# Kernel tuning notes

Measured on AMD Instinct MI355X. Metric: run time of the kernel, lower is better.

Reference implementation:

```python
import jax, jax.numpy as jnp
import numpy as np

B = 128
N = 512            # num_nodes
RU = 64            # rnn_units = hidden_size // num_nodes
IN_PER_NODE = 2    # input_size // num_nodes
MEM_DIM = 16
BOT_DIM = 4
IN_SZ = IN_PER_NODE + RU      # 66, concat(input, state) per node
OUT_SZ = 4 * RU               # 256, 4 LSTM gates


def setup_inputs() -> dict:
    key = jax.random.key(0)
    ks = jax.random.split(key, 12)
    std = 1.0 / np.sqrt(N * RU)  # reset_parameters: uniform(-std, std)
    u = lambda k, shape: jax.random.uniform(k, shape, jnp.float32, -std, std)
    return {
        "inputs": jax.random.normal(ks[0], (B, N * IN_PER_NODE), jnp.float32),
        "hx": jax.random.normal(ks[1], (B, N * RU), jnp.float32),
        "cx": jax.random.normal(ks[2], (B, N * RU), jnp.float32),
        "memory": u(ks[3], (N, MEM_DIM)),
        "w1": u(ks[4], (MEM_DIM, MEM_DIM)),
        "b1": u(ks[5], (MEM_DIM,)),
        "w2": u(ks[6], (MEM_DIM, BOT_DIM)),
        "b2": u(ks[7], (BOT_DIM,)),
        "w3": u(ks[8], (BOT_DIM, IN_SZ * OUT_SZ)),
        "b3": u(ks[9], (IN_SZ * OUT_SZ,)),
        "b_out": u(ks[10], (OUT_SZ,)),
    }


def reference(inputs, hx, cx, memory, w1, b1, w2, b2, w3, b3, b_out):
    b = inputs.shape[0]
    n = memory.shape[0]
    ru = hx.shape[1] // n
    # per-node concat of input and state: [B, N, IN_SZ]
    x = inputs.reshape(b, n, -1)
    h = hx.reshape(b, n, ru)
    xs = jnp.concatenate([x, h], axis=-1)
    # hypernetwork: memory -> per-node weight matrices [N, IN_SZ, OUT_SZ]
    mem = jnp.tanh(memory @ w1 + b1)
    mem = jnp.tanh(mem @ w2 + b2)
    W = (mem @ w3 + b3).reshape(n, xs.shape[-1], -1)
    # batched per-node matmul (original repeats W over batch; same math without the repeat)
    val = jax.nn.sigmoid(jnp.einsum('bni,nio->bno', xs, W)) + b_out  # [B, N, 4*RU]
    g = val.reshape(b, n, 4, ru)
    i_t = jax.nn.sigmoid(g[:, :, 0, :].reshape(b, n * ru))
    f_t = jax.nn.sigmoid(g[:, :, 1, :].reshape(b, n * ru))
    g_t = jnp.tanh(g[:, :, 2, :].reshape(b, n * ru))
    o_t = jax.nn.sigmoid(g[:, :, 3, :].reshape(b, n * ru))
    cy = cx * f_t + i_t * g_t
    hy = o_t * jnp.tanh(cy)
    return hy, cy
```

## Files before the change

### kernel.cpp

```cpp
#include <hip/hip_runtime.h>
#include <math.h>

#define BATCH 128
#define NNODE 512
#define RU 64
#define MEM_DIM 16
#define BOT_DIM 4
#define IN_SZ 66
#define OUT_SZ 256
#define HID (NNODE*RU)
#define W3_ROW 16896
#define W5F_FLOATS (240*512)
#define K_STEP 24576

typedef __attribute__((ext_vector_type(8))) short short8;
typedef __attribute__((ext_vector_type(4))) float float4v;

__device__ __forceinline__ unsigned short f2bf(float f) {
    unsigned int u = __float_as_uint(f);
    unsigned int r = (u + 0x7FFFu + ((u >> 16) & 1u)) >> 16;
    return (unsigned short)r;
}
__device__ __forceinline__ float fsig(float x) {
    return __builtin_amdgcn_rcpf(1.0f + __expf(-x));
}
__device__ __forceinline__ float ftanh(float x) {
    return 1.0f - 2.0f * __builtin_amdgcn_rcpf(1.0f + __expf(2.0f * x));
}

__global__ __launch_bounds__(256) void prep_kernel(
    const float* __restrict__ memory, const float* __restrict__ w1,
    const float* __restrict__ b1,     const float* __restrict__ w2,
    const float* __restrict__ b2,     const float* __restrict__ w3,
    const float* __restrict__ b3,     float* __restrict__ W5f,
    float* __restrict__ m2_ws)
{
    const int tid = threadIdx.x;
    const int bid = blockIdx.x;
    if (bid < 120) {
        const int id = bid * 256 + tid;
        const int F  = id * 4;
        const int f  = F >> 9;
        const int r  = F & 511;
        const int lane = r >> 3;
        const int j0   = r & 7;
        const int ks = f % 3;
        const int t2 = f / 3;
        const int ct = t2 & 15;
        const int k  = t2 >> 4;
        const int q = lane & 15, quad = lane >> 4;
        const int o = (ct & 3) * 64 + (ct >> 2) * 16 + q;
        const float* src = (k < 4) ? (w3 + k * W3_ROW) : b3;
        float4v v;
        #pragma unroll
        for (int jj = 0; jj < 4; ++jj) {
            const int s = ks * 32 + quad * 8 + j0 + jj;
            float x = 0.f;
            if (s < IN_SZ) {
                const int i = (s < 64) ? s + 2 : s - 64;
                x = src[i * OUT_SZ + o];
            }
            v[jj] = x;
        }
        *(float4v*)(W5f + F) = v;
    } else {
        const int n = (bid - 120) * 256 + tid;
        if (n < NNODE) {
            float memv[MEM_DIM];
            #pragma unroll
            for (int j = 0; j < MEM_DIM; ++j) memv[j] = memory[n * MEM_DIM + j];
            float mem1[MEM_DIM];
            #pragma unroll
            for (int t = 0; t < MEM_DIM; ++t) {
                float s = b1[t];
                #pragma unroll
                for (int j = 0; j < MEM_DIM; ++j) s += memv[j] * w1[j * MEM_DIM + t];
                mem1[t] = ftanh(s);
            }
            #pragma unroll
            for (int t = 0; t < BOT_DIM; ++t) {
                float s = b2[t];
                #pragma unroll
                for (int j = 0; j < MEM_DIM; ++j) s += mem1[j] * w2[j * BOT_DIM + t];
                m2_ws[n * 4 + t] = ftanh(s);
            }
        }
    }
}

__global__ __launch_bounds__(256, 3) void fused_kernel(
    const float* __restrict__ inputs, const float* __restrict__ hx,
    const float* __restrict__ cx,     const float* __restrict__ b_out,
    const float* __restrict__ W5f,    const float* __restrict__ m2_ws,
    float* __restrict__ out)
{
    __shared__ unsigned short Wl[24 * 512];
    const int tid  = threadIdx.x;
    const unsigned bid = blockIdx.x;
    const int n    = bid >> 1;
    const int h    = bid & 1;
    const int w    = tid >> 6;
    const int lane = tid & 63;
    const int q    = lane & 15;
    const int quad = lane >> 4;

    float coef[4];
    #pragma unroll
    for (int k = 0; k < 4; ++k) coef[k] = m2_ws[n * 4 + k];

    float4v xa[2][4];
    float xin[2][2];
    #pragma unroll
    for (int rt = 0; rt < 2; ++rt) {
        const int row = w * 32 + rt * 16 + q;
        const float* hrow = hx + (size_t)row * HID + n * RU + quad * 8;
        xa[rt][0] = *(const float4v*)(hrow);
        xa[rt][1] = *(const float4v*)(hrow + 4);
        xa[rt][2] = *(const float4v*)(hrow + 32);
        xa[rt][3] = *(const float4v*)(hrow + 36);
        if (quad == 0) {
            const float* ip = inputs + (size_t)row * (NNODE * 2) + n * 2;
            xin[rt][0] = ip[0];
            xin[rt][1] = ip[1];
        } else {
            xin[rt][0] = 0.f;
            xin[rt][1] = 0.f;
        }
    }

    #pragma unroll
    for (int it = 0; it < 6; ++it) {
        const int c  = it * 256 + tid;
        const int fl = c >> 6;
        const int l  = c & 63;
        const int ctl = fl / 3;
        const int ks  = fl - ctl * 3;
        const float* p = W5f + (size_t)(((h * 8 + ctl) * 3 + ks) * 512) + l * 8;
        float4v r0 = *(const float4v*)(p + 4 * K_STEP);
        float4v r1 = *(const float4v*)(p + 4 * K_STEP + 4);
        #pragma unroll
        for (int k = 0; k < 4; ++k) {
            r0 += coef[k] * *(const float4v*)(p + k * K_STEP);
            r1 += coef[k] * *(const float4v*)(p + k * K_STEP + 4);
        }
        short8 ov;
        ov[0] = (short)f2bf(r0[0]); ov[1] = (short)f2bf(r0[1]);
        ov[2] = (short)f2bf(r0[2]); ov[3] = (short)f2bf(r0[3]);
        ov[4] = (short)f2bf(r1[0]); ov[5] = (short)f2bf(r1[1]);
        ov[6] = (short)f2bf(r1[2]); ov[7] = (short)f2bf(r1[3]);
        *(short8*)(Wl + fl * 512 + l * 8) = ov;
    }

    float bo[2][4];
    #pragma unroll
    for (int rh = 0; rh < 2; ++rh)
        #pragma unroll
        for (int g = 0; g < 4; ++g)
            bo[rh][g] = b_out[g * 64 + (h * 2 + rh) * 16 + q];

    float cxr[2][4][2];
    #pragma unroll
    for (int rt = 0; rt < 2; ++rt)
        #pragma unroll
        for (int v = 0; v < 4; ++v) {
            const int b = w * 32 + rt * 16 + quad * 4 + v;
            #pragma unroll
            for (int rh = 0; rh < 2; ++rh)
                cxr[rt][v][rh] = cx[(size_t)b * HID + n * RU + (h * 2 + rh) * 16 + q];
        }

    short8 a[3][2];
    #pragma unroll
    for (int rt = 0; rt < 2; ++rt) {
        #pragma unroll
        for (int ksh = 0; ksh < 2; ++ksh) {
            float4v lo = xa[rt][ksh * 2];
            float4v hi = xa[rt][ksh * 2 + 1];
            short8 t;
            t[0] = (short)f2bf(lo[0]); t[1] = (short)f2bf(lo[1]);
            t[2] = (short)f2bf(lo[2]); t[3] = (short)f2bf(lo[3]);
            t[4] = (short)f2bf(hi[0]); t[5] = (short)f2bf(hi[1]);
            t[6] = (short)f2bf(hi[2]); t[7] = (short)f2bf(hi[3]);
            a[ksh][rt] = t;
        }
        short8 t2 = {0, 0, 0, 0, 0, 0, 0, 0};
        t2[0] = (short)f2bf(xin[rt][0]);
        t2[1] = (short)f2bf(xin[rt][1]);
        a[2][rt] = t2;
    }

    float4v acc[2][8];
    #pragma unroll
    for (int rt = 0; rt < 2; ++rt)
        #pragma unroll
        for (int ctl = 0; ctl < 8; ++ctl)
            acc[rt][ctl] = (float4v){0.f, 0.f, 0.f, 0.f};

    __syncthreads();

    #pragma unroll
    for (int ks = 0; ks < 3; ++ks) {
        #pragma unroll
        for (int ctl = 0; ctl < 8; ++ctl) {
            short8 bf = *(const short8*)(Wl + (ctl * 3 + ks) * 512 + lane * 8);
            acc[0][ctl] = __builtin_amdgcn_mfma_f32_16x16x32_bf16(a[ks][0], bf, acc[0][ctl], 0, 0, 0);
            acc[1][ctl] = __builtin_amdgcn_mfma_f32_16x16x32_bf16(a[ks][1], bf, acc[1][ctl], 0, 0, 0);
        }
    }

    #pragma unroll
    for (int rt = 0; rt < 2; ++rt) {
        #pragma unroll
        for (int v = 0; v < 4; ++v) {
            const int b = w * 32 + rt * 16 + quad * 4 + v;
            const size_t base = (size_t)b * HID + n * RU;
            #pragma unroll
            for (int rh = 0; rh < 2; ++rh) {
                float vi = fsig(acc[rt][rh * 4 + 0][v]) + bo[rh][0];
                float vf = fsig(acc[rt][rh * 4 + 1][v]) + bo[rh][1];
                float vg = fsig(acc[rt][rh * 4 + 2][v]) + bo[rh][2];
                float vo = fsig(acc[rt][rh * 4 + 3][v]) + bo[rh][3];
                float it = fsig(vi), ft = fsig(vf);
                float gt = ftanh(vg), ot = fsig(vo);
                const size_t idx = base + (h * 2 + rh) * 16 + q;
                float cc = cxr[rt][v][rh] * ft + it * gt;
                out[idx] = ot * ftanh(cc);
                out[(size_t)BATCH * HID + idx] = cc;
            }
        }
    }
}

extern "C" void kernel_launch(void* const* d_in, const int* in_sizes, int n_in,
                              void* d_out, int out_size, void* d_ws, size_t ws_size,
                              hipStream_t stream) {
    const float* inputs = (const float*)d_in[0];
    const float* hx     = (const float*)d_in[1];
    const float* cx     = (const float*)d_in[2];
    const float* memory = (const float*)d_in[3];
    const float* w1     = (const float*)d_in[4];
    const float* b1     = (const float*)d_in[5];
    const float* w2     = (const float*)d_in[6];
    const float* b2     = (const float*)d_in[7];
    const float* w3     = (const float*)d_in[8];
    const float* b3     = (const float*)d_in[9];
    const float* b_out  = (const float*)d_in[10];
    float* out = (float*)d_out;

    float* W5f   = (float*)d_ws;
    float* m2_ws = (float*)((char*)d_ws + W5F_FLOATS * 4);

    prep_kernel<<<122, 256, 0, stream>>>(memory, w1, b1, w2, b2, w3, b3, W5f, m2_ws);
    fused_kernel<<<NNODE * 2, 256, 0, stream>>>(inputs, hx, cx, b_out, W5f, m2_ws, out);
}
```

Measured before the change: 126.8 us.

## Precompute per-node bf16 weights in a separate kernel and async-load into LDS

Moves the hypernetwork weight combination out of the GEMM kernel into a dedicated kernel. That kernel writes fully materialized per-node bf16 weight matrices (512 x 24576 bf16, about 25 MB) to the workspace. The GEMM kernel then streams its half-tile straight into LDS with global_load_lds, replacing the 5-way fp32 loads and FMAs it did per block. It also swaps the manual bf16 rounding for packed bf16x2 conversion intrinsics and drops the occupancy hint. The tradeoff is a large extra global write and read of materialized weights, where before each GEMM block recomputed them from a small shared table.

```diff
diff --git a/kernel.cpp b/kernel.cpp
--- a/kernel.cpp
+++ b/kernel.cpp
@@ -1,4 +1,5 @@
 #include <hip/hip_runtime.h>
+#include <hip/hip_bf16.h>
 #include <math.h>
 
 #define BATCH 128
@@ -10,16 +11,16 @@
 #define OUT_SZ 256
 #define HID (NNODE*RU)
 #define W3_ROW 16896
-#define W5F_FLOATS (240*512)
-#define K_STEP 24576
+#define NODE_WC 24576
+#define HALF_WC 12288
 
 typedef __attribute__((ext_vector_type(8))) short short8;
 typedef __attribute__((ext_vector_type(4))) float float4v;
 
-__device__ __forceinline__ unsigned short f2bf(float f) {
-    unsigned int u = __float_as_uint(f);
-    unsigned int r = (u + 0x7FFFu + ((u >> 16) & 1u)) >> 16;
-    return (unsigned short)r;
+__device__ __forceinline__ unsigned pack2(float x, float y) {
+    union { __hip_bfloat162 h; unsigned u; } cv;
+    cv.h = __float22bfloat162_rn(make_float2(x, y));
+    return cv.u;
 }
 __device__ __forceinline__ float fsig(float x) {
     return __builtin_amdgcn_rcpf(1.0f + __expf(-x));
@@ -28,73 +29,86 @@
     return 1.0f - 2.0f * __builtin_amdgcn_rcpf(1.0f + __expf(2.0f * x));
 }
 
-__global__ __launch_bounds__(256) void prep_kernel(
+__global__ __launch_bounds__(256) void wcomb_kernel(
     const float* __restrict__ memory, const float* __restrict__ w1,
     const float* __restrict__ b1,     const float* __restrict__ w2,
     const float* __restrict__ b2,     const float* __restrict__ w3,
-    const float* __restrict__ b3,     float* __restrict__ W5f,
-    float* __restrict__ m2_ws)
+    const float* __restrict__ b3,     unsigned short* __restrict__ Wc)
 {
+    __shared__ alignas(16) float w5s[2][5][512];
+    __shared__ float mem1s[16][MEM_DIM];
+    __shared__ float m2s[16][BOT_DIM];
+
     const int tid = threadIdx.x;
-    const int bid = blockIdx.x;
-    if (bid < 120) {
-        const int id = bid * 256 + tid;
-        const int F  = id * 4;
-        const int f  = F >> 9;
-        const int r  = F & 511;
-        const int lane = r >> 3;
-        const int j0   = r & 7;
+    const unsigned bid = blockIdx.x;
+    const int fp = bid >> 5;
+    const int ng = bid & 31;
+
+    for (int e = tid; e < 5120; e += 256) {
+        const int fl  = e / 2560;
+        const int k   = (e - fl * 2560) >> 9;
+        const int idx = e & 511;
+        const int l = idx >> 3, j = idx & 7;
+        const int f  = fp * 2 + fl;
         const int ks = f % 3;
-        const int t2 = f / 3;
-        const int ct = t2 & 15;
-        const int k  = t2 >> 4;
-        const int q = lane & 15, quad = lane >> 4;
+        const int ct = f / 3;
+        const int q = l & 15, quad = l >> 4;
         const int o = (ct & 3) * 64 + (ct >> 2) * 16 + q;
-        const float* src = (k < 4) ? (w3 + k * W3_ROW) : b3;
-        float4v v;
-        #pragma unroll
-        for (int jj = 0; jj < 4; ++jj) {
-            const int s = ks * 32 + quad * 8 + j0 + jj;
-            float x = 0.f;
-            if (s < IN_SZ) {
-                const int i = (s < 64) ? s + 2 : s - 64;
-                x = src[i * OUT_SZ + o];
-            }
-            v[jj] = x;
-        }
-        *(float4v*)(W5f + F) = v;
-    } else {
-        const int n = (bid - 120) * 256 + tid;
-        if (n < NNODE) {
-            float memv[MEM_DIM];
-            #pragma unroll
-            for (int j = 0; j < MEM_DIM; ++j) memv[j] = memory[n * MEM_DIM + j];
-            float mem1[MEM_DIM];
-            #pragma unroll
-            for (int t = 0; t < MEM_DIM; ++t) {
-                float s = b1[t];
-                #pragma unroll
-                for (int j = 0; j < MEM_DIM; ++j) s += memv[j] * w1[j * MEM_DIM + t];
-                mem1[t] = ftanh(s);
-            }
-            #pragma unroll
-            for (int t = 0; t < BOT_DIM; ++t) {
-                float s = b2[t];
-                #pragma unroll
-                for (int j = 0; j < MEM_DIM; ++j) s += mem1[j] * w2[j * BOT_DIM + t];
-                m2_ws[n * 4 + t] = ftanh(s);
-            }
-        }
-    }
-}
-
-__global__ __launch_bounds__(256, 3) void fused_kernel(
+        const int s = ks * 32 + quad * 8 + j;
+        float v = 0.f;
+        if (s < IN_SZ) {
+            const int i = (s < 64) ? s + 2 : s - 64;
+            v = (k < 4) ? w3[k * W3_ROW + i * OUT_SZ + o] : b3[i * OUT_SZ + o];
+        }
+        w5s[fl][k][idx] = v;
+    }
+
+    {
+        const int nn = tid >> 4, t = tid & 15;
+        float s = b1[t];
+        #pragma unroll
+        for (int j = 0; j < MEM_DIM; ++j)
+            s += memory[(ng * 16 + nn) * MEM_DIM + j] * w1[j * MEM_DIM + t];
+        mem1s[nn][t] = ftanh(s);
+    }
+    __syncthreads();
+    if (tid < 64) {
+        const int nn = tid >> 2, t4 = tid & 3;
+        float s = b2[t4];
+        #pragma unroll
+        for (int j = 0; j < MEM_DIM; ++j)
+            s += mem1s[nn][j] * w2[j * BOT_DIM + t4];
+        m2s[nn][t4] = ftanh(s);
+    }
+    __syncthreads();
+
+    const int fl   = tid >> 7;
+    const int idx4 = (tid & 127) * 4;
+    const float4v wk0 = *(const float4v*)&w5s[fl][0][idx4];
+    const float4v wk1 = *(const float4v*)&w5s[fl][1][idx4];
+    const float4v wk2 = *(const float4v*)&w5s[fl][2][idx4];
+    const float4v wk3 = *(const float4v*)&w5s[fl][3][idx4];
+    const float4v wb  = *(const float4v*)&w5s[fl][4][idx4];
+
+    unsigned short* base = Wc + (size_t)(ng * 16) * NODE_WC
+                         + (fp * 2 + fl) * 512 + idx4;
+    #pragma unroll 4
+    for (int nn = 0; nn < 16; ++nn) {
+        float4v r = wb + m2s[nn][0] * wk0 + m2s[nn][1] * wk1
+                       + m2s[nn][2] * wk2 + m2s[nn][3] * wk3;
+        uint2 p;
+        p.x = pack2(r[0], r[1]);
+        p.y = pack2(r[2], r[3]);
+        *(uint2*)(base + (size_t)nn * NODE_WC) = p;
+    }
+}
+
+__global__ __launch_bounds__(256) void gemm_kernel(
     const float* __restrict__ inputs, const float* __restrict__ hx,
     const float* __restrict__ cx,     const float* __restrict__ b_out,
-    const float* __restrict__ W5f,    const float* __restrict__ m2_ws,
-    float* __restrict__ out)
+    const unsigned short* __restrict__ Wc, float* __restrict__ out)
 {
-    __shared__ unsigned short Wl[24 * 512];
+    __shared__ unsigned short Wl[HALF_WC];
     const int tid  = threadIdx.x;
     const unsigned bid = blockIdx.x;
     const int n    = bid >> 1;
@@ -104,9 +118,13 @@
     const int q    = lane & 15;
     const int quad = lane >> 4;
 
-    float coef[4];
-    #pragma unroll
-    for (int k = 0; k < 4; ++k) coef[k] = m2_ws[n * 4 + k];
+    const unsigned short* gW = Wc + (size_t)n * NODE_WC + h * HALF_WC;
+    for (int t = w; t < 24; t += 4) {
+        __builtin_amdgcn_global_load_lds(
+            (__attribute__((address_space(1))) void*)(gW + t * 512 + lane * 8),
+            (__attribute__((address_space(3))) void*)(Wl + t * 512),
+            16, 0, 0);
+    }
 
     float4v xa[2][4];
     float xin[2][2];
@@ -128,29 +146,6 @@
         }
     }
 
-    #pragma unroll
-    for (int it = 0; it < 6; ++it) {
-        const int c  = it * 256 + tid;
-        const int fl = c >> 6;
-        const int l  = c & 63;
-        const int ctl = fl / 3;
-        const int ks  = fl - ctl * 3;
-        const float* p = W5f + (size_t)(((h * 8 + ctl) * 3 + ks) * 512) + l * 8;
-        float4v r0 = *(const float4v*)(p + 4 * K_STEP);
-        float4v r1 = *(const float4v*)(p + 4 * K_STEP + 4);
-        #pragma unroll
-        for (int k = 0; k < 4; ++k) {
-            r0 += coef[k] * *(const float4v*)(p + k * K_STEP);
-            r1 += coef[k] * *(const float4v*)(p + k * K_STEP + 4);
-        }
-        short8 ov;
-        ov[0] = (short)f2bf(r0[0]); ov[1] = (short)f2bf(r0[1]);
-        ov[2] = (short)f2bf(r0[2]); ov[3] = (short)f2bf(r0[3]);
-        ov[4] = (short)f2bf(r1[0]); ov[5] = (short)f2bf(r1[1]);
-        ov[6] = (short)f2bf(r1[2]); ov[7] = (short)f2bf(r1[3]);
-        *(short8*)(Wl + fl * 512 + l * 8) = ov;
-    }
-
     float bo[2][4];
     #pragma unroll
     for (int rh = 0; rh < 2; ++rh)
@@ -176,17 +171,17 @@
         for (int ksh = 0; ksh < 2; ++ksh) {
             float4v lo = xa[rt][ksh * 2];
             float4v hi = xa[rt][ksh * 2 + 1];
-            short8 t;
-            t[0] = (short)f2bf(lo[0]); t[1] = (short)f2bf(lo[1]);
-            t[2] = (short)f2bf(lo[2]); t[3] = (short)f2bf(lo[3]);
-            t[4] = (short)f2bf(hi[0]); t[5] = (short)f2bf(hi[1]);
-            t[6] = (short)f2bf(hi[2]); t[7] = (short)f2bf(hi[3]);
-            a[ksh][rt] = t;
-        }
-        short8 t2 = {0, 0, 0, 0, 0, 0, 0, 0};
-        t2[0] = (short)f2bf(xin[rt][0]);
-        t2[1] = (short)f2bf(xin[rt][1]);
-        a[2][rt] = t2;
+            union { short8 s; unsigned u[4]; } t;
+            t.u[0] = pack2(lo[0], lo[1]);
+            t.u[1] = pack2(lo[2], lo[3]);
+            t.u[2] = pack2(hi[0], hi[1]);
+            t.u[3] = pack2(hi[2], hi[3]);
+            a[ksh][rt] = t.s;
+        }
+        union { short8 s; unsigned u[4]; } t2;
+        t2.u[0] = pack2(xin[rt][0], xin[rt][1]);
+        t2.u[1] = t2.u[2] = t2.u[3] = 0u;
+        a[2][rt] = t2.s;
     }
 
     float4v acc[2][8];
@@ -247,9 +242,8 @@
     const float* b_out  = (const float*)d_in[10];
     float* out = (float*)d_out;
 
-    float* W5f   = (float*)d_ws;
-    float* m2_ws = (float*)((char*)d_ws + W5F_FLOATS * 4);
-
-    prep_kernel<<<122, 256, 0, stream>>>(memory, w1, b1, w2, b2, w3, b3, W5f, m2_ws);
-    fused_kernel<<<NNODE * 2, 256, 0, stream>>>(inputs, hx, cx, b_out, W5f, m2_ws, out);
-}
+    unsigned short* Wc = (unsigned short*)d_ws;
+
+    wcomb_kernel<<<24 * 32, 256, 0, stream>>>(memory, w1, b1, w2, b2, w3, b3, Wc);
+    gemm_kernel<<<NNODE * 2, 256, 0, stream>>>(inputs, hx, cx, b_out, Wc, out);
+}
```

Result: slower. 131.3 us (+3.6%).

## Process both output halves per block with fp16 weight table and staged overlap

Applied to the files above, without the earlier changes.

Each block now handles a whole node instead of half a node, so hx is loaded and converted once per node rather than twice. The second half's weight generation and cx loads are interleaved with the first half's MFMA work and epilogue, using double-buffered LDS. The precomputed hypernetwork table is stored in fp16 instead of fp32, and the per-node weight combination is done with packed fp16 math, which halves table traffic but reduces accumulation precision. The grid halves to 512 blocks, which lowers parallelism and raises register and LDS use per block.

```diff
diff --git a/kernel.cpp b/kernel.cpp
--- a/kernel.cpp
+++ b/kernel.cpp
@@ -10,17 +10,12 @@
 #define OUT_SZ 256
 #define HID (NNODE*RU)
 #define W3_ROW 16896
-#define W5F_FLOATS (240*512)
-#define K_STEP 24576
-
-typedef __attribute__((ext_vector_type(8))) short short8;
+#define TAB_HALVES (240*512)
+#define KSTEP (48*512)
+
+typedef _Float16 half8 __attribute__((ext_vector_type(8)));
 typedef __attribute__((ext_vector_type(4))) float float4v;
 
-__device__ __forceinline__ unsigned short f2bf(float f) {
-    unsigned int u = __float_as_uint(f);
-    unsigned int r = (u + 0x7FFFu + ((u >> 16) & 1u)) >> 16;
-    return (unsigned short)r;
-}
 __device__ __forceinline__ float fsig(float x) {
     return __builtin_amdgcn_rcpf(1.0f + __expf(-x));
 }
@@ -32,39 +27,36 @@
     const float* __restrict__ memory, const float* __restrict__ w1,
     const float* __restrict__ b1,     const float* __restrict__ w2,
     const float* __restrict__ b2,     const float* __restrict__ w3,
-    const float* __restrict__ b3,     float* __restrict__ W5f,
+    const float* __restrict__ b3,     _Float16* __restrict__ tab,
     float* __restrict__ m2_ws)
 {
     const int tid = threadIdx.x;
     const int bid = blockIdx.x;
-    if (bid < 120) {
-        const int id = bid * 256 + tid;
-        const int F  = id * 4;
-        const int f  = F >> 9;
-        const int r  = F & 511;
-        const int lane = r >> 3;
-        const int j0   = r & 7;
-        const int ks = f % 3;
-        const int t2 = f / 3;
-        const int ct = t2 & 15;
-        const int k  = t2 >> 4;
-        const int q = lane & 15, quad = lane >> 4;
+    if (bid < 60) {
+        const int c = bid * 256 + tid;
+        const int f = c >> 6;
+        const int l = c & 63;
+        const int k   = f / 48;
+        const int rem = f - k * 48;
+        const int ct  = rem / 3;
+        const int ks  = rem - ct * 3;
+        const int q = l & 15, quad = l >> 4;
         const int o = (ct & 3) * 64 + (ct >> 2) * 16 + q;
         const float* src = (k < 4) ? (w3 + k * W3_ROW) : b3;
-        float4v v;
-        #pragma unroll
-        for (int jj = 0; jj < 4; ++jj) {
-            const int s = ks * 32 + quad * 8 + j0 + jj;
+        half8 v;
+        #pragma unroll
+        for (int j = 0; j < 8; ++j) {
+            const int s = ks * 32 + quad * 8 + j;
             float x = 0.f;
             if (s < IN_SZ) {
                 const int i = (s < 64) ? s + 2 : s - 64;
                 x = src[i * OUT_SZ + o];
             }
-            v[jj] = x;
-        }
-        *(float4v*)(W5f + F) = v;
+            v[j] = (_Float16)x;
+        }
+        *(half8*)(tab + f * 512 + l * 8) = v;
     } else {
-        const int n = (bid - 120) * 256 + tid;
+        const int n = (bid - 60) * 256 + tid;
         if (n < NNODE) {
             float memv[MEM_DIM];
             #pragma unroll
@@ -88,25 +80,27 @@
     }
 }
 
-__global__ __launch_bounds__(256, 3) void fused_kernel(
+__global__ __launch_bounds__(256) void fused_kernel(
     const float* __restrict__ inputs, const float* __restrict__ hx,
     const float* __restrict__ cx,     const float* __restrict__ b_out,
-    const float* __restrict__ W5f,    const float* __restrict__ m2_ws,
+    const _Float16* __restrict__ tab, const float* __restrict__ m2_ws,
     float* __restrict__ out)
 {
-    __shared__ unsigned short Wl[24 * 512];
+    __shared__ _Float16 Wl[2][24 * 512];
     const int tid  = threadIdx.x;
-    const unsigned bid = blockIdx.x;
-    const int n    = bid >> 1;
-    const int h    = bid & 1;
+    const int n    = blockIdx.x;
     const int w    = tid >> 6;
     const int lane = tid & 63;
     const int q    = lane & 15;
     const int quad = lane >> 4;
 
-    float coef[4];
-    #pragma unroll
-    for (int k = 0; k < 4; ++k) coef[k] = m2_ws[n * 4 + k];
+    const float4v m2v = *(const float4v*)(m2_ws + n * 4);
+    half8 vc[4];
+    #pragma unroll
+    for (int k = 0; k < 4; ++k) {
+        const _Float16 c = (_Float16)m2v[k];
+        vc[k] = (half8){c, c, c, c, c, c, c, c};
+    }
 
     float4v xa[2][4];
     float xin[2][2];
@@ -128,37 +122,93 @@
         }
     }
 
+    float bo[2][2][4];
+    #pragma unroll
+    for (int h = 0; h < 2; ++h)
+        #pragma unroll
+        for (int rh = 0; rh < 2; ++rh)
+            #pragma unroll
+            for (int g = 0; g < 4; ++g)
+                bo[h][rh][g] = b_out[g * 64 + (h * 2 + rh) * 16 + q];
+
+    float cx0[2][4][2];
+    #pragma unroll
+    for (int rt = 0; rt < 2; ++rt)
+        #pragma unroll
+        for (int v = 0; v < 4; ++v) {
+            const int b = w * 32 + rt * 16 + quad * 4 + v;
+            #pragma unroll
+            for (int rh = 0; rh < 2; ++rh)
+                cx0[rt][v][rh] = cx[(size_t)b * HID + n * RU + rh * 16 + q];
+        }
+
     #pragma unroll
     for (int it = 0; it < 6; ++it) {
         const int c  = it * 256 + tid;
         const int fl = c >> 6;
         const int l  = c & 63;
-        const int ctl = fl / 3;
-        const int ks  = fl - ctl * 3;
-        const float* p = W5f + (size_t)(((h * 8 + ctl) * 3 + ks) * 512) + l * 8;
-        float4v r0 = *(const float4v*)(p + 4 * K_STEP);
-        float4v r1 = *(const float4v*)(p + 4 * K_STEP + 4);
-        #pragma unroll
-        for (int k = 0; k < 4; ++k) {
-            r0 += coef[k] * *(const float4v*)(p + k * K_STEP);
-            r1 += coef[k] * *(const float4v*)(p + k * K_STEP + 4);
-        }
-        short8 ov;
-        ov[0] = (short)f2bf(r0[0]); ov[1] = (short)f2bf(r0[1]);
-        ov[2] = (short)f2bf(r0[2]); ov[3] = (short)f2bf(r0[3]);
-        ov[4] = (short)f2bf(r1[0]); ov[5] = (short)f2bf(r1[1]);
-        ov[6] = (short)f2bf(r1[2]); ov[7] = (short)f2bf(r1[3]);
-        *(short8*)(Wl + fl * 512 + l * 8) = ov;
-    }
-
-    float bo[2][4];
-    #pragma unroll
-    for (int rh = 0; rh < 2; ++rh)
-        #pragma unroll
-        for (int g = 0; g < 4; ++g)
-            bo[rh][g] = b_out[g * 64 + (h * 2 + rh) * 16 + q];
-
-    float cxr[2][4][2];
+        const _Float16* p = tab + (0 * 24 + fl) * 512 + l * 8;
+        half8 r = *(const half8*)(p + 4 * KSTEP);
+        r += vc[0] * *(const half8*)(p);
+        r += vc[1] * *(const half8*)(p + KSTEP);
+        r += vc[2] * *(const half8*)(p + 2 * KSTEP);
+        r += vc[3] * *(const half8*)(p + 3 * KSTEP);
+        *(half8*)(&Wl[0][fl * 512 + l * 8]) = r;
+    }
+
+    half8 a[3][2];
+    #pragma unroll
+    for (int rt = 0; rt < 2; ++rt) {
+        #pragma unroll
+        for (int ksh = 0; ksh < 2; ++ksh) {
+            const float4v lo = xa[rt][ksh * 2];
+            const float4v hi = xa[rt][ksh * 2 + 1];
+            half8 t;
+            t[0] = (_Float16)lo[0]; t[1] = (_Float16)lo[1];
+            t[2] = (_Float16)lo[2]; t[3] = (_Float16)lo[3];
+            t[4] = (_Float16)hi[0]; t[5] = (_Float16)hi[1];
+            t[6] = (_Float16)hi[2]; t[7] = (_Float16)hi[3];
+            a[ksh][rt] = t;
+        }
+        half8 t2 = (half8){0, 0, 0, 0, 0, 0, 0, 0};
+        t2[0] = (_Float16)xin[rt][0];
+        t2[1] = (_Float16)xin[rt][1];
+        a[2][rt] = t2;
+    }
+
+    float4v acc[2][8];
+    #pragma unroll
+    for (int rt = 0; rt < 2; ++rt)
+        #pragma unroll
+        for (int ctl = 0; ctl < 8; ++ctl)
+            acc[rt][ctl] = (float4v){0.f, 0.f, 0.f, 0.f};
+
+    __syncthreads();
+
+    #pragma unroll
+    for (int ks = 0; ks < 3; ++ks)
+        #pragma unroll
+        for (int ctl = 0; ctl < 8; ++ctl) {
+            const half8 bf = *(const half8*)(&Wl[0][(ctl * 3 + ks) * 512 + lane * 8]);
+            acc[0][ctl] = __builtin_amdgcn_mfma_f32_16x16x32_f16(a[ks][0], bf, acc[0][ctl], 0, 0, 0);
+            acc[1][ctl] = __builtin_amdgcn_mfma_f32_16x16x32_f16(a[ks][1], bf, acc[1][ctl], 0, 0, 0);
+        }
+
+    #pragma unroll
+    for (int it = 0; it < 6; ++it) {
+        const int c  = it * 256 + tid;
+        const int fl = c >> 6;
+        const int l  = c & 63;
+        const _Float16* p = tab + (24 + fl) * 512 + l * 8;
+        half8 r = *(const half8*)(p + 4 * KSTEP);
+        r += vc[0] * *(const half8*)(p);
+        r += vc[1] * *(const half8*)(p + KSTEP);
+        r += vc[2] * *(const half8*)(p + 2 * KSTEP);
+        r += vc[3] * *(const half8*)(p + 3 * KSTEP);
+        *(half8*)(&Wl[1][fl * 512 + l * 8]) = r;
+    }
+
+    float cx1[2][4][2];
     #pragma unroll
     for (int rt = 0; rt < 2; ++rt)
         #pragma unroll
@@ -166,30 +216,27 @@
             const int b = w * 32 + rt * 16 + quad * 4 + v;
             #pragma unroll
             for (int rh = 0; rh < 2; ++rh)
-                cxr[rt][v][rh] = cx[(size_t)b * HID + n * RU + (h * 2 + rh) * 16 + q];
-        }
-
-    short8 a[3][2];
-    #pragma unroll
-    for (int rt = 0; rt < 2; ++rt) {
-        #pragma unroll
-        for (int ksh = 0; ksh < 2; ++ksh) {
-            float4v lo = xa[rt][ksh * 2];
-            float4v hi = xa[rt][ksh * 2 + 1];
-            short8 t;
-            t[0] = (short)f2bf(lo[0]); t[1] = (short)f2bf(lo[1]);
-            t[2] = (short)f2bf(lo[2]); t[3] = (short)f2bf(lo[3]);
-            t[4] = (short)f2bf(hi[0]); t[5] = (short)f2bf(hi[1]);
-            t[6] = (short)f2bf(hi[2]); t[7] = (short)f2bf(hi[3]);
-            a[ksh][rt] = t;
-        }
-        short8 t2 = {0, 0, 0, 0, 0, 0, 0, 0};
-        t2[0] = (short)f2bf(xin[rt][0]);
-        t2[1] = (short)f2bf(xin[rt][1]);
-        a[2][rt] = t2;
-    }
-
-    float4v acc[2][8];
+                cx1[rt][v][rh] = cx[(size_t)b * HID + n * RU + 32 + rh * 16 + q];
+        }
+
+    float hy0[2][4][2], cy0[2][4][2];
+    #pragma unroll
+    for (int rt = 0; rt < 2; ++rt)
+        #pragma unroll
+        for (int v = 0; v < 4; ++v)
+            #pragma unroll
+            for (int rh = 0; rh < 2; ++rh) {
+                float vi = fsig(acc[rt][rh * 4 + 0][v]) + bo[0][rh][0];
+                float vf = fsig(acc[rt][rh * 4 + 1][v]) + bo[0][rh][1];
+                float vg = fsig(acc[rt][rh * 4 + 2][v]) + bo[0][rh][2];
+                float vo = fsig(acc[rt][rh * 4 + 3][v]) + bo[0][rh][3];
+                float it = fsig(vi), ft = fsig(vf);
+                float gt = ftanh(vg), ot = fsig(vo);
+                float cc = cx0[rt][v][rh] * ft + it * gt;
+                hy0[rt][v][rh] = ot * ftanh(cc);
+                cy0[rt][v][rh] = cc;
+            }
+
     #pragma unroll
     for (int rt = 0; rt < 2; ++rt)
         #pragma unroll
@@ -199,36 +246,48 @@
     __syncthreads();
 
     #pragma unroll
-    for (int ks = 0; ks < 3; ++ks) {
-        #pragma unroll
-        for (int ctl = 0; ctl < 8; ++ctl) {
-            short8 bf = *(const short8*)(Wl + (ctl * 3 + ks) * 512 + lane * 8);
-            acc[0][ctl] = __builtin_amdgcn_mfma_f32_16x16x32_bf16(a[ks][0], bf, acc[0][ctl], 0, 0, 0);
-            acc[1][ctl] = __builtin_amdgcn_mfma_f32_16x16x32_bf16(a[ks][1], bf, acc[1][ctl], 0, 0, 0);
-        }
-    }
-
-    #pragma unroll
-    for (int rt = 0; rt < 2; ++rt) {
+    for (int rt = 0; rt < 2; ++rt)
         #pragma unroll
         for (int v = 0; v < 4; ++v) {
             const int b = w * 32 + rt * 16 + quad * 4 + v;
             const size_t base = (size_t)b * HID + n * RU;
             #pragma unroll
             for (int rh = 0; rh < 2; ++rh) {
-                float vi = fsig(acc[rt][rh * 4 + 0][v]) + bo[rh][0];
-                float vf = fsig(acc[rt][rh * 4 + 1][v]) + bo[rh][1];
-                float vg = fsig(acc[rt][rh * 4 + 2][v]) + bo[rh][2];
-                float vo = fsig(acc[rt][rh * 4 + 3][v]) + bo[rh][3];
+                const size_t idx = base + rh * 16 + q;
+                out[idx] = hy0[rt][v][rh];
+                out[(size_t)BATCH * HID + idx] = cy0[rt][v][rh];
+            }
+        }
+
+    #pragma unroll
+    for (int ks = 0; ks < 3; ++ks)
+        #pragma unroll
+        for (int ctl = 0; ctl < 8; ++ctl) {
+            const half8 bf = *(const half8*)(&Wl[1][(ctl * 3 + ks) * 512 + lane * 8]);
+            acc[0][ctl] = __builtin_amdgcn_mfma_f32_16x16x32_f16(a[ks][0], bf, acc[0][ctl], 0, 0, 0);
+            acc[1][ctl] = __builtin_amdgcn_mfma_f32_16x16x32_f16(a[ks][1], bf, acc[1][ctl], 0, 0, 0);
+        }
+
+    #pragma unroll
+    for (int rt = 0; rt < 2; ++rt)
+        #pragma unroll
+        for (int v = 0; v < 4; ++v) {
+            const int b = w * 32 + rt * 16 + quad * 4 + v;
+            const size_t base = (size_t)b * HID + n * RU;
+            #pragma unroll
+            for (int rh = 0; rh < 2; ++rh) {
+                float vi = fsig(acc[rt][rh * 4 + 0][v]) + bo[1][rh][0];
+                float vf = fsig(acc[rt][rh * 4 + 1][v]) + bo[1][rh][1];
+                float vg = fsig(acc[rt][rh * 4 + 2][v]) + bo[1][rh][2];
+                float vo = fsig(acc[rt][rh * 4 + 3][v]) + bo[1][rh][3];
                 float it = fsig(vi), ft = fsig(vf);
                 float gt = ftanh(vg), ot = fsig(vo);
-                const size_t idx = base + (h * 2 + rh) * 16 + q;
-                float cc = cxr[rt][v][rh] * ft + it * gt;
+                float cc = cx1[rt][v][rh] * ft + it * gt;
+                const size_t idx = base + 32 + rh * 16 + q;
                 out[idx] = ot * ftanh(cc);
                 out[(size_t)BATCH * HID + idx] = cc;
             }
         }
-    }
 }
 
 extern "C" void kernel_launch(void* const* d_in, const int* in_sizes, int n_in,
@@ -247,9 +306,9 @@
     const float* b_out  = (const float*)d_in[10];
     float* out = (float*)d_out;
 
-    float* W5f   = (float*)d_ws;
-    float* m2_ws = (float*)((char*)d_ws + W5F_FLOATS * 4);
-
-    prep_kernel<<<122, 256, 0, stream>>>(memory, w1, b1, w2, b2, w3, b3, W5f, m2_ws);
-    fused_kernel<<<NNODE * 2, 256, 0, stream>>>(inputs, hx, cx, b_out, W5f, m2_ws, out);
-}
+    _Float16* tab = (_Float16*)d_ws;
+    float* m2_ws  = (float*)((char*)d_ws + TAB_HALVES * 2);
+
+    prep_kernel<<<62, 256, 0, stream>>>(memory, w1, b1, w2, b2, w3, b3, tab, m2_ws);
+    fused_kernel<<<NNODE, 256, 0, stream>>>(inputs, hx, cx, b_out, tab, m2_ws, out);
+}
```

New measurement: 122.1 us. -3.7%, faster.
